# Kernel optimization log

Measured on AMD Instinct MI355X. Metric: run time of the kernel, lower is better.

## Reference

```python
import jax, jax.numpy as jnp
import numpy as np

# ---- Build Cayley tables for projective GA G(3,0,1), basis ordered by grade ----
_BLADES = [(), (0,), (1,), (2,), (3,), (0,1), (0,2), (0,3), (1,2), (1,3), (2,3),
           (0,1,2), (0,1,3), (0,2,3), (1,2,3), (0,1,2,3)]
_IDX = {b: i for i, b in enumerate(_BLADES)}

def _blade_mul(a, b, metric):
    """Multiply basis blades a*b. Returns (sign, result_blade); sign=0 if it vanishes."""
    arr = list(a) + list(b)
    sign = 1
    changed = True
    while changed:
        changed = False
        for i in range(len(arr) - 1):
            if arr[i] > arr[i + 1]:
                arr[i], arr[i + 1] = arr[i + 1], arr[i]
                sign = -sign
                changed = True
            elif arr[i] == arr[i + 1]:
                sign *= metric[arr[i]]
                del arr[i:i + 2]
                changed = True
                break
    return sign, tuple(arr)

def _build_tables():
    metric = [0, 1, 1, 1]  # e0^2 = 0 (degenerate), e1^2=e2^2=e3^2=1
    G = np.zeros((16, 16, 16), np.float32)  # geometric product
    W = np.zeros((16, 16, 16), np.float32)  # outer (wedge) product
    for a in _BLADES:
        for b in _BLADES:
            s, r = _blade_mul(a, b, metric)
            if s != 0:
                G[_IDX[a], _IDX[b], _IDX[r]] = s
            if not (set(a) & set(b)):
                s2, r2 = _blade_mul(a, b, [1, 1, 1, 1])
                W[_IDX[a], _IDX[b], _IDX[r2]] = s2
    # Right-complement dual: dual(e_a) = s * e_c with e_a ^ dual(e_a) = e0123
    full = (0, 1, 2, 3)
    dual_idx = np.zeros(16, np.int32)
    dual_sign = np.zeros(16, np.float32)
    for a in _BLADES:
        c = tuple(sorted(set(full) - set(a)))
        s, _ = _blade_mul(a, c, [1, 1, 1, 1])
        dual_idx[_IDX[a]] = _IDX[c]
        dual_sign[_IDX[a]] = s
    # Coefficient map: dual(x)[j] = dual_sign[dual_idx[j]] * x[dual_idx[j]]
    out_sign = dual_sign[dual_idx]
    return jnp.asarray(G), jnp.asarray(W), jnp.asarray(dual_idx), jnp.asarray(out_sign)

_G, _W, _DUAL_IDX, _DUAL_SIGN = _build_tables()
_PSS = 15  # index of pseudoscalar e0123

def _dual(x):
    return x[..., _DUAL_IDX] * _DUAL_SIGN


def setup_inputs() -> dict:
    key = jax.random.key(0)
    k1, k2, k3 = jax.random.split(key, 3)
    B, T, C = 64, 8192, 16
    return {
        "x": jax.random.normal(k1, (B, T, C), dtype=jnp.float32),
        "y": jax.random.normal(k2, (B, T, C), dtype=jnp.float32),
        "ref": jax.random.normal(k3, (B, T, C), dtype=jnp.float32),
    }


def reference(x, y, ref):
    # Geometric product over the Cayley table
    gp = jnp.einsum("bti,btj,ijk->btk", x, y, _G)
    # E(3)-equivariant join: ref_e0123 * dual(dual(x) ^ dual(y))
    wedge = jnp.einsum("bti,btj,ijk->btk", _dual(x), _dual(y), _W)
    join = ref[..., _PSS:_PSS + 1] * _dual(wedge)
    return jnp.concatenate([gp, join], axis=-1)  # (B, T, 32)
```

## Files before the change

kernel.cpp:

```cpp
#include <hip/hip_runtime.h>

namespace ga {

constexpr int MASK[16]        = {0,1,2,4,8,3,5,9,6,10,12,7,11,13,14,15};
constexpr int IDX_OF_MASK[16] = {0,1,2,5,3,6,8,11,4,7,9,12,10,13,14,15};

constexpr int popc(int v) { int c = 0; while (v) { c += v & 1; v >>= 1; } return c; }

constexpr int reorder_sign(int a, int b) {
    int s = 0; int t = a >> 1;
    while (t) { s += popc(t & b); t >>= 1; }
    return (s & 1) ? -1 : 1;
}

struct Term { signed char i, j, k, s; };

struct GPTab { Term t[192]; };
constexpr GPTab build_gp() {
    GPTab T{}; int n = 0;
    for (int i = 0; i < 16; i++)
        for (int j = 0; j < 16; j++) {
            int a = MASK[i], b = MASK[j];
            if (a & b & 1) continue;
            T.t[n].i = (signed char)i;
            T.t[n].j = (signed char)j;
            T.t[n].k = (signed char)IDX_OF_MASK[a ^ b];
            T.t[n].s = (signed char)reorder_sign(a, b);
            n++;
        }
    return T;
}

struct JNTab { Term t[81]; };
constexpr JNTab build_join() {
    JNTab T{}; int n = 0;
    int didx[16] = {}, dsgn[16] = {};
    for (int i = 0; i < 16; i++) {
        int a = MASK[i], c = (~a) & 0xF;
        didx[i] = IDX_OF_MASK[c];
        dsgn[i] = reorder_sign(a, c);
    }
    for (int i = 0; i < 16; i++)
        for (int j = 0; j < 16; j++) {
            int p = didx[i], q = didx[j];
            int a = MASK[p], b = MASK[q];
            if (a & b) continue;
            int m = IDX_OF_MASK[a | b];
            int k = didx[m];
            int s = dsgn[i] * dsgn[j] * dsgn[m] * reorder_sign(a, b);
            T.t[n].i = (signed char)i;
            T.t[n].j = (signed char)j;
            T.t[n].k = (signed char)k;
            T.t[n].s = (signed char)s;
            n++;
        }
    return T;
}

constexpr GPTab G = build_gp();
constexpr JNTab J = build_join();

}


typedef const __attribute__((address_space(1))) void* gas_ptr;
typedef __attribute__((address_space(3))) void*       las_ptr;

constexpr int NITER = 4;

template<int HALF>
__device__ __forceinline__ void accum_half(const float* __restrict__ xx,
                                           const float* __restrict__ yy,
                                           float* __restrict__ acc,
                                           float* __restrict__ jacc)
{
#pragma unroll
    for (int t = 0; t < 192; t++) {
        const int tk = ga::G.t[t].k;
        if ((tk < 8) != (HALF == 0)) continue;
        const float v = xx[ga::G.t[t].i] * yy[ga::G.t[t].j];
        if (ga::G.t[t].s > 0) acc[tk & 7] += v; else acc[tk & 7] -= v;
    }
#pragma unroll
    for (int t = 0; t < 81; t++) {
        const int tk = ga::J.t[t].k;
        if ((tk < 8) != (HALF == 0)) continue;
        const float v = xx[ga::J.t[t].i] * yy[ga::J.t[t].j];
        if (ga::J.t[t].s > 0) jacc[tk & 7] += v; else jacc[tk & 7] -= v;
    }
}

__global__ __launch_bounds__(128, 4)
void MVGeometricBilinear_kernel(const float* __restrict__ x,
                                const float* __restrict__ y,
                                const float* __restrict__ ref,
                                float* __restrict__ out,
                                int nchunks, int gstride)
{
    __shared__ __align__(16) float buf[2][2048];

    const int tid  = threadIdx.x;
    const int lane = tid & 63;
    const int wid  = tid >> 6;

    const long chunk0 = blockIdx.x;
    if (chunk0 >= nchunks) return;

    float rr[NITER];
    {
        long c = chunk0;
#pragma unroll
        for (int it = 0; it < NITER; ++it) {
            if (c < nchunks) rr[it] = ref[(c * 64 + lane) * 16 + 15];
            c += gstride;
        }
    }

    int srcoff[4];
    int fragoff[4];
#pragma unroll
    for (int k = 0; k < 4; ++k) {
        const int slot = k * 64 + lane;
        const int j = ((slot & 3) - ((slot >> 3) & 3)) & 3;
        srcoff[k] = (slot & ~3) | j;
        const int s = (k + ((lane >> 1) & 3)) & 3;
        fragoff[k] = lane * 16 + (s << 2);
    }

    const float4* gsrc = reinterpret_cast<const float4*>(wid ? y : x);
    const int ldsbase = wid ? 1024 : 0;

    auto dma = [&](long c, int b) {
#pragma unroll
        for (int k = 0; k < 4; ++k)
            __builtin_amdgcn_global_load_lds(
                (gas_ptr)(gsrc + c * 256 + srcoff[k]),
                (las_ptr)(&buf[b][ldsbase + k * 256]), 16, 0, 0);
    };

    long chunk = chunk0;
    int cur = 0;
    dma(chunk, 0);

#pragma unroll
    for (int it = 0; it < NITER; ++it) {
        const long next = chunk + gstride;
        const bool pf = (it + 1 < NITER) && (next < nchunks);
        if (pf) dma(next, cur ^ 1);

        if (it == 0) {
            if (pf) asm volatile("s_waitcnt vmcnt(4)" ::: "memory");
            else    asm volatile("s_waitcnt vmcnt(0)" ::: "memory");
        } else {
            if (pf) asm volatile("s_waitcnt vmcnt(8)" ::: "memory");
            else    asm volatile("s_waitcnt vmcnt(4)" ::: "memory");
        }
        __builtin_amdgcn_s_barrier();

        float xx[16], yy[16];
#pragma unroll
        for (int k = 0; k < 4; ++k) {
            const float4 vx = *reinterpret_cast<const float4*>(&buf[cur][fragoff[k]]);
            const float4 vy = *reinterpret_cast<const float4*>(&buf[cur][1024 + fragoff[k]]);
            xx[4*k+0] = vx.x; xx[4*k+1] = vx.y; xx[4*k+2] = vx.z; xx[4*k+3] = vx.w;
            yy[4*k+0] = vy.x; yy[4*k+1] = vy.y; yy[4*k+2] = vy.z; yy[4*k+3] = vy.w;
        }
        asm volatile("s_waitcnt lgkmcnt(0)" ::: "memory");
        __builtin_amdgcn_s_barrier();

        float acc[8]  = {0.f,0.f,0.f,0.f,0.f,0.f,0.f,0.f};
        float jacc[8] = {0.f,0.f,0.f,0.f,0.f,0.f,0.f,0.f};
        if (wid == 0) accum_half<0>(xx, yy, acc, jacc);
        else          accum_half<1>(xx, yy, acc, jacc);
        const float r = rr[it];

        {
            float* lo = &buf[cur][0];
            const int pb = lane * 32, px = lane & 7;
            const int qg = 2 * wid, qj = 4 + 2 * wid;
            *reinterpret_cast<float4*>(lo + pb + (((qg    ) ^ px) << 2)) =
                make_float4(acc[0], acc[1], acc[2], acc[3]);
            *reinterpret_cast<float4*>(lo + pb + (((qg + 1) ^ px) << 2)) =
                make_float4(acc[4], acc[5], acc[6], acc[7]);
            *reinterpret_cast<float4*>(lo + pb + (((qj    ) ^ px) << 2)) =
                make_float4(r*jacc[0], r*jacc[1], r*jacc[2], r*jacc[3]);
            *reinterpret_cast<float4*>(lo + pb + (((qj + 1) ^ px) << 2)) =
                make_float4(r*jacc[4], r*jacc[5], r*jacc[6], r*jacc[7]);
        }
        asm volatile("s_waitcnt lgkmcnt(0)" ::: "memory");
        __builtin_amdgcn_s_barrier();

        {
            float4* go = reinterpret_cast<float4*>(out) + chunk * 512;
#pragma unroll
            for (int c = 0; c < 4; ++c) {
                const int g = c * 128 + wid * 64 + lane;
                const int p = g >> 3, q = g & 7;
                go[g] = *reinterpret_cast<const float4*>(
                            &buf[cur][p * 32 + ((q ^ (p & 7)) << 2)]);
            }
        }
        asm volatile("s_waitcnt lgkmcnt(0)" ::: "memory");
        __builtin_amdgcn_s_barrier();

        if (!pf) break;
        cur ^= 1;
        chunk = next;
    }
}

__global__ __launch_bounds__(64)
void MVGeometricBilinear_tail(const float* __restrict__ x,
                              const float* __restrict__ y,
                              const float* __restrict__ ref,
                              float* __restrict__ out,
                              int start, int npts)
{
    int pt = start + blockIdx.x * 64 + threadIdx.x;
    if (pt >= npts) return;
    float xx[16], yy[16];
#pragma unroll
    for (int k = 0; k < 16; k++) { xx[k] = x[(size_t)pt*16+k]; yy[k] = y[(size_t)pt*16+k]; }
    const float r = ref[(size_t)pt*16+15];
    float gp[16] = {}, jn[16] = {};
#pragma unroll
    for (int t = 0; t < 192; t++) {
        const float v = xx[ga::G.t[t].i] * yy[ga::G.t[t].j];
        if (ga::G.t[t].s > 0) gp[ga::G.t[t].k] += v; else gp[ga::G.t[t].k] -= v;
    }
#pragma unroll
    for (int t = 0; t < 81; t++) {
        const float v = xx[ga::J.t[t].i] * yy[ga::J.t[t].j];
        if (ga::J.t[t].s > 0) jn[ga::J.t[t].k] += v; else jn[ga::J.t[t].k] -= v;
    }
#pragma unroll
    for (int k = 0; k < 16; k++) out[(size_t)pt*32+k] = gp[k];
#pragma unroll
    for (int k = 0; k < 16; k++) out[(size_t)pt*32+16+k] = r * jn[k];
}

extern "C" void kernel_launch(void* const* d_in, const int* in_sizes, int n_in,
                              void* d_out, int out_size, void* d_ws, size_t ws_size,
                              hipStream_t stream) {
    const float* x   = (const float*)d_in[0];
    const float* y   = (const float*)d_in[1];
    const float* ref = (const float*)d_in[2];
    float* out = (float*)d_out;

    const int npts    = in_sizes[0] / 16;
    const int nchunks = npts / 64;

    if (nchunks > 0) {
        int blocks = nchunks < 2560 ? nchunks : 2560;
        const int need = (nchunks + NITER - 1) / NITER;
        if (blocks < need) blocks = need;
        MVGeometricBilinear_kernel<<<blocks, 128, 0, stream>>>(
            x, y, ref, out, nchunks, blocks);
    }

    const int rem = npts - nchunks * 64;
    if (rem > 0) {
        MVGeometricBilinear_tail<<<(rem + 63) / 64, 64, 0, stream>>>(
            x, y, ref, out, nchunks * 64, npts);
    }
}
```

Before: 147.6 us.

## Collapse two-wave block into single-wave block and drop all barriers

Each block now has one 64-lane wave instead of two. That wave loads both x and y tiles through global_load_lds and computes all 16 geometric-product and 16 join outputs per point, rather than splitting the output halves across two waves. Because one wave owns the whole tile, every s_barrier is removed, and the vmcnt waits are doubled to match the extra loads. In exchange, each wave does twice the arithmetic and needs more registers, and with the same grid there are half as many waves per CU to hide memory latency.

```diff
diff --git a/kernel.cpp b/kernel.cpp
--- a/kernel.cpp
+++ b/kernel.cpp
@@ -68,29 +68,7 @@
 
 constexpr int NITER = 4;
 
-template<int HALF>
-__device__ __forceinline__ void accum_half(const float* __restrict__ xx,
-                                           const float* __restrict__ yy,
-                                           float* __restrict__ acc,
-                                           float* __restrict__ jacc)
-{
-#pragma unroll
-    for (int t = 0; t < 192; t++) {
-        const int tk = ga::G.t[t].k;
-        if ((tk < 8) != (HALF == 0)) continue;
-        const float v = xx[ga::G.t[t].i] * yy[ga::G.t[t].j];
-        if (ga::G.t[t].s > 0) acc[tk & 7] += v; else acc[tk & 7] -= v;
-    }
-#pragma unroll
-    for (int t = 0; t < 81; t++) {
-        const int tk = ga::J.t[t].k;
-        if ((tk < 8) != (HALF == 0)) continue;
-        const float v = xx[ga::J.t[t].i] * yy[ga::J.t[t].j];
-        if (ga::J.t[t].s > 0) jacc[tk & 7] += v; else jacc[tk & 7] -= v;
-    }
-}
-
-__global__ __launch_bounds__(128, 4)
+__global__ __launch_bounds__(64, 2)
 void MVGeometricBilinear_kernel(const float* __restrict__ x,
                                 const float* __restrict__ y,
                                 const float* __restrict__ ref,
@@ -99,10 +77,7 @@
 {
     __shared__ __align__(16) float buf[2][2048];
 
-    const int tid  = threadIdx.x;
-    const int lane = tid & 63;
-    const int wid  = tid >> 6;
-
+    const int lane = threadIdx.x;
     const long chunk0 = blockIdx.x;
     if (chunk0 >= nchunks) return;
 
@@ -127,15 +102,18 @@
         fragoff[k] = lane * 16 + (s << 2);
     }
 
-    const float4* gsrc = reinterpret_cast<const float4*>(wid ? y : x);
-    const int ldsbase = wid ? 1024 : 0;
+    const float4* gx = reinterpret_cast<const float4*>(x);
+    const float4* gy = reinterpret_cast<const float4*>(y);
 
     auto dma = [&](long c, int b) {
 #pragma unroll
         for (int k = 0; k < 4; ++k)
-            __builtin_amdgcn_global_load_lds(
-                (gas_ptr)(gsrc + c * 256 + srcoff[k]),
-                (las_ptr)(&buf[b][ldsbase + k * 256]), 16, 0, 0);
+            __builtin_amdgcn_global_load_lds((gas_ptr)(gx + c * 256 + srcoff[k]),
+                                             (las_ptr)(&buf[b][k * 256]), 16, 0, 0);
+#pragma unroll
+        for (int k = 0; k < 4; ++k)
+            __builtin_amdgcn_global_load_lds((gas_ptr)(gy + c * 256 + srcoff[k]),
+                                             (las_ptr)(&buf[b][1024 + k * 256]), 16, 0, 0);
     };
 
     long chunk = chunk0;
@@ -149,13 +127,12 @@
         if (pf) dma(next, cur ^ 1);
 
         if (it == 0) {
-            if (pf) asm volatile("s_waitcnt vmcnt(4)" ::: "memory");
+            if (pf) asm volatile("s_waitcnt vmcnt(8)" ::: "memory");
             else    asm volatile("s_waitcnt vmcnt(0)" ::: "memory");
         } else {
-            if (pf) asm volatile("s_waitcnt vmcnt(8)" ::: "memory");
-            else    asm volatile("s_waitcnt vmcnt(4)" ::: "memory");
-        }
-        __builtin_amdgcn_s_barrier();
+            if (pf) asm volatile("s_waitcnt vmcnt(16)" ::: "memory");
+            else    asm volatile("s_waitcnt vmcnt(8)" ::: "memory");
+        }
 
         float xx[16], yy[16];
 #pragma unroll
@@ -165,43 +142,50 @@
             xx[4*k+0] = vx.x; xx[4*k+1] = vx.y; xx[4*k+2] = vx.z; xx[4*k+3] = vx.w;
             yy[4*k+0] = vy.x; yy[4*k+1] = vy.y; yy[4*k+2] = vy.z; yy[4*k+3] = vy.w;
         }
+        const float r = rr[it];
+
+        float gp[16] = {0.f,0.f,0.f,0.f,0.f,0.f,0.f,0.f,
+                        0.f,0.f,0.f,0.f,0.f,0.f,0.f,0.f};
+        float jn[16] = {0.f,0.f,0.f,0.f,0.f,0.f,0.f,0.f,
+                        0.f,0.f,0.f,0.f,0.f,0.f,0.f,0.f};
+#pragma unroll
+        for (int t = 0; t < 192; t++) {
+            const int ti = ga::G.t[t].i, tj = ga::G.t[t].j, tk = ga::G.t[t].k;
+            const float v = xx[ti] * yy[tj];
+            if (ga::G.t[t].s > 0) gp[tk] += v; else gp[tk] -= v;
+        }
+#pragma unroll
+        for (int t = 0; t < 81; t++) {
+            const int ti = ga::J.t[t].i, tj = ga::J.t[t].j, tk = ga::J.t[t].k;
+            const float v = xx[ti] * yy[tj];
+            if (ga::J.t[t].s > 0) jn[tk] += v; else jn[tk] -= v;
+        }
+
+        asm volatile("" ::: "memory");
+
+        float* lo = &buf[cur][0];
+        const int px = lane & 7;
+#pragma unroll
+        for (int q = 0; q < 4; q++)
+            *reinterpret_cast<float4*>(lo + lane * 32 + ((q ^ px) << 2)) =
+                make_float4(gp[4*q+0], gp[4*q+1], gp[4*q+2], gp[4*q+3]);
+#pragma unroll
+        for (int q = 0; q < 4; q++)
+            *reinterpret_cast<float4*>(lo + lane * 32 + (((q + 4) ^ px) << 2)) =
+                make_float4(r*jn[4*q+0], r*jn[4*q+1], r*jn[4*q+2], r*jn[4*q+3]);
+
         asm volatile("s_waitcnt lgkmcnt(0)" ::: "memory");
-        __builtin_amdgcn_s_barrier();
-
-        float acc[8]  = {0.f,0.f,0.f,0.f,0.f,0.f,0.f,0.f};
-        float jacc[8] = {0.f,0.f,0.f,0.f,0.f,0.f,0.f,0.f};
-        if (wid == 0) accum_half<0>(xx, yy, acc, jacc);
-        else          accum_half<1>(xx, yy, acc, jacc);
-        const float r = rr[it];
-
-        {
-            float* lo = &buf[cur][0];
-            const int pb = lane * 32, px = lane & 7;
-            const int qg = 2 * wid, qj = 4 + 2 * wid;
-            *reinterpret_cast<float4*>(lo + pb + (((qg    ) ^ px) << 2)) =
-                make_float4(acc[0], acc[1], acc[2], acc[3]);
-            *reinterpret_cast<float4*>(lo + pb + (((qg + 1) ^ px) << 2)) =
-                make_float4(acc[4], acc[5], acc[6], acc[7]);
-            *reinterpret_cast<float4*>(lo + pb + (((qj    ) ^ px) << 2)) =
-                make_float4(r*jacc[0], r*jacc[1], r*jacc[2], r*jacc[3]);
-            *reinterpret_cast<float4*>(lo + pb + (((qj + 1) ^ px) << 2)) =
-                make_float4(r*jacc[4], r*jacc[5], r*jacc[6], r*jacc[7]);
-        }
-        asm volatile("s_waitcnt lgkmcnt(0)" ::: "memory");
-        __builtin_amdgcn_s_barrier();
-
-        {
-            float4* go = reinterpret_cast<float4*>(out) + chunk * 512;
-#pragma unroll
-            for (int c = 0; c < 4; ++c) {
-                const int g = c * 128 + wid * 64 + lane;
-                const int p = g >> 3, q = g & 7;
-                go[g] = *reinterpret_cast<const float4*>(
-                            &buf[cur][p * 32 + ((q ^ (p & 7)) << 2)]);
-            }
-        }
-        asm volatile("s_waitcnt lgkmcnt(0)" ::: "memory");
-        __builtin_amdgcn_s_barrier();
+
+        float4* go = reinterpret_cast<float4*>(out) + chunk * 512;
+#pragma unroll
+        for (int c = 0; c < 8; c++) {
+            const int g = c * 64 + lane;
+            const int p = g >> 3, q = g & 7;
+            go[g] = *reinterpret_cast<const float4*>(
+                        lo + p * 32 + ((q ^ (p & 7)) << 2));
+        }
+
+        asm volatile("" ::: "memory");
 
         if (!pf) break;
         cur ^= 1;
@@ -254,7 +238,7 @@
         int blocks = nchunks < 2560 ? nchunks : 2560;
         const int need = (nchunks + NITER - 1) / NITER;
         if (blocks < need) blocks = need;
-        MVGeometricBilinear_kernel<<<blocks, 128, 0, stream>>>(
+        MVGeometricBilinear_kernel<<<blocks, 64, 0, stream>>>(
             x, y, ref, out, nchunks, blocks);
     }
 
```

Result: no change. 147.2 us (-0.3%).
